# Performance work log

Measured on AMD Instinct MI355X. Metric: run time of the kernel, lower is better.

The kernel has to match this reference:

```python
import jax, jax.numpy as jnp
import numpy as np

N = 100000
E = 1600000
VOCAB = 16
D = 128   # node_embedding_dim == hidden_channels
NUM_LAYERS = 3


def setup_inputs() -> dict:
    key = jax.random.key(0)
    ks = jax.random.split(key, 12)
    x = jax.random.randint(ks[0], (N, 1), 0, VOCAB, dtype=jnp.int64) if jax.config.jax_enable_x64 else jax.random.randint(ks[0], (N, 1), 0, VOCAB, dtype=jnp.int32)
    edge_index = jax.random.randint(ks[1], (2, E), 0, N, dtype=jnp.int32)
    s = 1.0 / np.sqrt(D)
    inp = {
        "x": x,
        "edge_index": edge_index,
        "emb": jax.random.normal(ks[2], (VOCAB, D), jnp.float32),
        "W0": jax.random.normal(ks[3], (D, D), jnp.float32) * s,
        "b0": jnp.zeros((D,), jnp.float32),
        "W1": jax.random.normal(ks[4], (D, D), jnp.float32) * s,
        "b1": jnp.zeros((D,), jnp.float32),
        "W2": jax.random.normal(ks[5], (D, D), jnp.float32) * s,
        "b2": jnp.zeros((D,), jnp.float32),
        "Wm1": jax.random.normal(ks[6], (2 * D, D), jnp.float32) * (1.0 / np.sqrt(2 * D)),
        "bm1": jnp.zeros((D,), jnp.float32),
        "Wm2": jax.random.normal(ks[7], (D, 3), jnp.float32) * s,
        "bm2": jnp.zeros((3,), jnp.float32),
    }
    return inp


def _gcn_conv(h, src_sl, dst_sl, norm, W, b):
    # PyG GCNConv: x' = scatter_dst(norm * (x W)[src]) + b, with self-loops included
    hW = h @ W                                   # [N, D]
    msg = hW[src_sl] * norm[:, None]             # [(E+N), D] gather
    agg = jax.ops.segment_sum(msg, dst_sl, num_segments=N)  # scatter-add
    return agg + b


def reference(x, edge_index, emb, W0, b0, W1, b1, W2, b2, Wm1, bm1, Wm2, bm2):
    src, dst = edge_index[0], edge_index[1]
    # add self-loops
    loop = jnp.arange(N, dtype=src.dtype)
    src_sl = jnp.concatenate([src, loop])
    dst_sl = jnp.concatenate([dst, loop])
    # symmetric degree normalization: deg counted on dst (col)
    deg = jax.ops.segment_sum(jnp.ones_like(dst_sl, jnp.float32), dst_sl, num_segments=N)
    dis = jnp.where(deg > 0, jax.lax.rsqrt(jnp.maximum(deg, 1.0)), 0.0)
    norm = dis[src_sl] * dis[dst_sl]             # [(E+N)]

    # node encoder: embedding lookup (dropout omitted: eval mode)
    h = emb[x[:, 0]]                             # [N, D]
    for W, b in ((W0, b0), (W1, b1), (W2, b2)):
        h = jax.nn.relu(_gcn_conv(h, src_sl, dst_sl, norm, W, b))

    # edge classifier: gather endpoints, concat, MLP
    ef = jnp.concatenate([h[src], h[dst]], axis=-1)   # [E, 2D]
    hid = jax.nn.relu(ef @ Wm1 + bm1)
    return hid @ Wm2 + bm2                             # [E, 3]
```

## Files before the change

kernel.cpp:

```cpp
#include <hip/hip_runtime.h>
#include <hip/hip_bf16.h>

#define N_NODES 100000
#define N_EDGES 1600000


__global__ void zero_cnt_k(int* cnt, int n) {
    int i = blockIdx.x * 256 + threadIdx.x;
    if (i < n) cnt[i] = 0;
}

__global__ void hist_k(const int* __restrict__ ei, int* __restrict__ cnt, int E) {
    int e = blockIdx.x * 256 + threadIdx.x;
    if (e < E) atomicAdd(&cnt[ei[E + e]], 1);
}

__global__ void dis_k(const int* __restrict__ cnt, const int* __restrict__ x,
                      float* __restrict__ dis, float2* __restrict__ sx, int n) {
    int i = blockIdx.x * 256 + threadIdx.x;
    if (i < n) {
        float d = rsqrtf(1.0f + (float)cnt[i]);
        dis[i] = d;
        sx[i] = make_float2(d, __int_as_float(x[i]));
    }
}

__global__ void scan_cnt_k(const int* __restrict__ cnt, int* __restrict__ offs,
                           int* __restrict__ bsum, int n) {
    __shared__ int buf[2][256];
    int t = threadIdx.x;
    int i = blockIdx.x * 256 + t;
    int v = (i < n) ? cnt[i] : 0;
    int p = 0;
    buf[0][t] = v;
    __syncthreads();
    for (int off = 1; off < 256; off <<= 1) {
        int nv = buf[p][t];
        if (t >= off) nv += buf[p][t - off];
        buf[p ^ 1][t] = nv;
        p ^= 1;
        __syncthreads();
    }
    if (i < n) offs[i] = buf[p][t] - v;
    if (t == 255) bsum[blockIdx.x] = buf[p][t];
}

__global__ void scan_bsum_k(int* __restrict__ bsum, int nb) {
    __shared__ int buf[2][512];
    int t = threadIdx.x;
    int v = (t < nb) ? bsum[t] : 0;
    int p = 0;
    buf[0][t] = v;
    __syncthreads();
    for (int off = 1; off < 512; off <<= 1) {
        int nv = buf[p][t];
        if (t >= off) nv += buf[p][t - off];
        buf[p ^ 1][t] = nv;
        p ^= 1;
        __syncthreads();
    }
    if (t < nb) bsum[t] = buf[p][t] - v;
}

__global__ void scan_add_k(int* __restrict__ offs, int* __restrict__ cursor,
                           const int* __restrict__ bsum, int n, int total) {
    int i = blockIdx.x * 256 + threadIdx.x;
    if (i < n) {
        int o = offs[i] + bsum[blockIdx.x];
        offs[i] = o;
        cursor[i] = o;
    }
    if (i == 0) offs[n] = total;
}

__global__ void fill_csr_k(const int* __restrict__ ei, int* __restrict__ cursor,
                           int* __restrict__ srcs, int* __restrict__ eid, int E) {
    int e = blockIdx.x * 256 + threadIdx.x;
    if (e < E) {
        int s = ei[e];
        int d = ei[E + e];
        int pos = atomicAdd(&cursor[d], 1);
        srcs[pos] = s;
        eid[pos] = e;
    }
}


__global__ void t0_k(const float* __restrict__ emb, const float* __restrict__ W0,
                     float* __restrict__ T0) {
    int v = blockIdx.x;
    int c = threadIdx.x;
    float acc = 0.f;
    for (int k = 0; k < 128; ++k) acc += emb[v * 128 + k] * W0[k * 128 + c];
    T0[v * 128 + c] = acc;
}

__global__ __launch_bounds__(256) void vgather_k(const float2* __restrict__ sx,
                                                 const int* __restrict__ offs,
                                                 const int* __restrict__ srcs,
                                                 const float* __restrict__ dis,
                                                 const int* __restrict__ x,
                                                 const float* __restrict__ T0,
                                                 const float* __restrict__ b0,
                                                 float* __restrict__ h, int n) {
    __shared__ float t0s[16 * 128];
    __shared__ float cv[4][16];
    int t = threadIdx.x;
    #pragma unroll
    for (int i = 0; i < 8; ++i) t0s[t + i * 256] = T0[t + i * 256];
    if (t < 64) cv[t >> 4][t & 15] = 0.f;
    __syncthreads();

    int w = t >> 6, lane = t & 63;
    int node = blockIdx.x * 4 + w;
    float di = dis[node];
    int j0 = offs[node], j1 = offs[node + 1];
    for (int j = j0 + lane; j < j1; j += 64) {
        float2 v = sx[srcs[j]];
        atomicAdd(&cv[w][__float_as_int(v.y)], v.x);
    }
    if (lane == 0) atomicAdd(&cv[w][x[node]], di);
    __syncthreads();

    float2 acc = make_float2(0.f, 0.f);
    #pragma unroll
    for (int v = 0; v < 16; ++v) {
        float c = cv[w][v];
        float2 tv = *(const float2*)&t0s[v * 128 + lane * 2];
        acc.x += c * tv.x;
        acc.y += c * tv.y;
    }
    float2 bb = *(const float2*)&b0[lane * 2];
    float2 r = make_float2(fmaxf(di * acc.x + bb.x, 0.f),
                           fmaxf(di * acc.y + bb.y, 0.f));
    ((float2*)h)[(size_t)node * 64 + lane] = r;
}


__global__ __launch_bounds__(256) void matmul128_k(const float* __restrict__ in,
                                                   const float* __restrict__ W,
                                                   float* __restrict__ out,
                                                   const float* __restrict__ scale,
                                                   int n) {
    __shared__ float hlds[64][132];
    int t = threadIdx.x;
    int row0 = blockIdx.x * 64;
    #pragma unroll
    for (int it = 0; it < 8; ++it) {
        int i4 = t + it * 256;
        int r = i4 >> 5, c4 = (i4 & 31) << 2;
        float4 v = make_float4(0.f, 0.f, 0.f, 0.f);
        int g = row0 + r;
        if (g < n) v = *(const float4*)&in[(size_t)g * 128 + c4];
        *(float4*)&hlds[r][c4] = v;
    }
    __syncthreads();
    int cg = t & 31, rg = t >> 5;
    int c0 = cg << 2;
    float acc[8][4];
    #pragma unroll
    for (int r = 0; r < 8; ++r)
        for (int j = 0; j < 4; ++j) acc[r][j] = 0.f;
    #pragma unroll 4
    for (int k = 0; k < 128; ++k) {
        float4 w = *(const float4*)&W[(size_t)k * 128 + c0];
        #pragma unroll
        for (int r = 0; r < 8; ++r) {
            float hk = hlds[rg * 8 + r][k];
            acc[r][0] += hk * w.x;
            acc[r][1] += hk * w.y;
            acc[r][2] += hk * w.z;
            acc[r][3] += hk * w.w;
        }
    }
    #pragma unroll
    for (int r = 0; r < 8; ++r) {
        int g = row0 + rg * 8 + r;
        if (g < n) {
            float sc = scale[g];
            float4 o = make_float4(acc[r][0] * sc, acc[r][1] * sc,
                                   acc[r][2] * sc, acc[r][3] * sc);
            *(float4*)&out[(size_t)g * 128 + c0] = o;
        }
    }
}

__global__ __launch_bounds__(256) void matmulAB_k(const float* __restrict__ in,
                                                  const float* __restrict__ WA,
                                                  const float* __restrict__ WB,
                                                  float* __restrict__ outA,
                                                  float* __restrict__ outB, int n) {
    __shared__ float hlds[64][132];
    int t = threadIdx.x;
    int row0 = blockIdx.x * 64;
    #pragma unroll
    for (int it = 0; it < 8; ++it) {
        int i4 = t + it * 256;
        int r = i4 >> 5, c4 = (i4 & 31) << 2;
        float4 v = make_float4(0.f, 0.f, 0.f, 0.f);
        int g = row0 + r;
        if (g < n) v = *(const float4*)&in[(size_t)g * 128 + c4];
        *(float4*)&hlds[r][c4] = v;
    }
    __syncthreads();
    int cg = t & 31, rg = t >> 5;
    int c0 = cg << 2;
    float accA[8][4], accB[8][4];
    #pragma unroll
    for (int r = 0; r < 8; ++r)
        for (int j = 0; j < 4; ++j) { accA[r][j] = 0.f; accB[r][j] = 0.f; }
    #pragma unroll 2
    for (int k = 0; k < 128; ++k) {
        float4 wa = *(const float4*)&WA[(size_t)k * 128 + c0];
        float4 wb = *(const float4*)&WB[(size_t)k * 128 + c0];
        #pragma unroll
        for (int r = 0; r < 8; ++r) {
            float hk = hlds[rg * 8 + r][k];
            accA[r][0] += hk * wa.x;
            accA[r][1] += hk * wa.y;
            accA[r][2] += hk * wa.z;
            accA[r][3] += hk * wa.w;
            accB[r][0] += hk * wb.x;
            accB[r][1] += hk * wb.y;
            accB[r][2] += hk * wb.z;
            accB[r][3] += hk * wb.w;
        }
    }
    #pragma unroll
    for (int r = 0; r < 8; ++r) {
        int g = row0 + rg * 8 + r;
        if (g < n) {
            *(float4*)&outA[(size_t)g * 128 + c0] = *(float4*)&accA[r][0];
            *(float4*)&outB[(size_t)g * 128 + c0] = *(float4*)&accB[r][0];
        }
    }
}

__global__ __launch_bounds__(256) void gcn_gather_k(const float* __restrict__ hW,
                                                    const int* __restrict__ offs,
                                                    const int* __restrict__ srcs,
                                                    const float* __restrict__ dis,
                                                    const float* __restrict__ bias,
                                                    float* __restrict__ hout, int n) {
    int t = threadIdx.x;
    int node = blockIdx.x * 4 + (t >> 6);
    int lane = t & 63;
    int g = lane >> 4, sl = lane & 15;
    const float4* hw4 = (const float4*)hW;
    float4 a0 = make_float4(0.f, 0.f, 0.f, 0.f), a1 = a0;
    if (g == 0) {
        size_t rb = (size_t)node * 32 + sl * 2;
        a0 = hw4[rb];
        a1 = hw4[rb + 1];
    }
    int j0 = offs[node], j1 = offs[node + 1];
    for (int j = j0 + g; j < j1; j += 4) {
        size_t rb = (size_t)srcs[j] * 32 + sl * 2;
        float4 u0 = hw4[rb], u1 = hw4[rb + 1];
        a0.x += u0.x; a0.y += u0.y; a0.z += u0.z; a0.w += u0.w;
        a1.x += u1.x; a1.y += u1.y; a1.z += u1.z; a1.w += u1.w;
    }
    #pragma unroll
    for (int m = 16; m <= 32; m <<= 1) {
        a0.x += __shfl_xor(a0.x, m); a0.y += __shfl_xor(a0.y, m);
        a0.z += __shfl_xor(a0.z, m); a0.w += __shfl_xor(a0.w, m);
        a1.x += __shfl_xor(a1.x, m); a1.y += __shfl_xor(a1.y, m);
        a1.z += __shfl_xor(a1.z, m); a1.w += __shfl_xor(a1.w, m);
    }
    if (g == 0) {
        float di = dis[node];
        float4 bb0 = *(const float4*)&bias[sl * 8];
        float4 bb1 = *(const float4*)&bias[sl * 8 + 4];
        float4 r0 = make_float4(fmaxf(di * a0.x + bb0.x, 0.f),
                                fmaxf(di * a0.y + bb0.y, 0.f),
                                fmaxf(di * a0.z + bb0.z, 0.f),
                                fmaxf(di * a0.w + bb0.w, 0.f));
        float4 r1 = make_float4(fmaxf(di * a1.x + bb1.x, 0.f),
                                fmaxf(di * a1.y + bb1.y, 0.f),
                                fmaxf(di * a1.z + bb1.z, 0.f),
                                fmaxf(di * a1.w + bb1.w, 0.f));
        size_t rb = (size_t)node * 32 + sl * 2;
        ((float4*)hout)[rb] = r0;
        ((float4*)hout)[rb + 1] = r1;
    }
}

__global__ __launch_bounds__(256) void edge_mlp_k(const int* __restrict__ offs,
                                                  const int* __restrict__ srcs,
                                                  const int* __restrict__ eid,
                                                  const float* __restrict__ A,
                                                  const float* __restrict__ B,
                                                  const float* __restrict__ Wm2,
                                                  const float* __restrict__ bm1,
                                                  const float* __restrict__ bm2,
                                                  float* __restrict__ out, int n) {
    int t = threadIdx.x;
    int node = blockIdx.x * 4 + (t >> 6);
    int lane = t & 63;
    int g = lane >> 4, sl = lane & 15;
    int j0 = offs[node], j1 = offs[node + 1];
    if (j0 == j1) return;

    const float4* B4 = (const float4*)(B + (size_t)node * 128 + sl * 8);
    const float4* bm14 = (const float4*)(bm1 + sl * 8);
    float4 pre0 = B4[0], pre1 = B4[1];
    float4 m0 = bm14[0], m1 = bm14[1];
    pre0.x += m0.x; pre0.y += m0.y; pre0.z += m0.z; pre0.w += m0.w;
    pre1.x += m1.x; pre1.y += m1.y; pre1.z += m1.z; pre1.w += m1.w;

    float wv[8][3];
    #pragma unroll
    for (int i = 0; i < 8; ++i) {
        int f = sl * 8 + i;
        wv[i][0] = Wm2[f * 3 + 0];
        wv[i][1] = Wm2[f * 3 + 1];
        wv[i][2] = Wm2[f * 3 + 2];
    }
    float c0 = bm2[0], c1 = bm2[1], c2 = bm2[2];

    for (int jb = j0; jb < j1; jb += 4) {
        int jj = jb + g;
        bool act = jj < j1;
        int jsafe = act ? jj : j0;
        int s = srcs[jsafe];
        int e = eid[jsafe];
        const float4* A4 = (const float4*)(A + (size_t)s * 128 + sl * 8);
        float4 a0 = A4[0], a1 = A4[1];
        float h[8];
        h[0] = fmaxf(a0.x + pre0.x, 0.f);
        h[1] = fmaxf(a0.y + pre0.y, 0.f);
        h[2] = fmaxf(a0.z + pre0.z, 0.f);
        h[3] = fmaxf(a0.w + pre0.w, 0.f);
        h[4] = fmaxf(a1.x + pre1.x, 0.f);
        h[5] = fmaxf(a1.y + pre1.y, 0.f);
        h[6] = fmaxf(a1.z + pre1.z, 0.f);
        h[7] = fmaxf(a1.w + pre1.w, 0.f);
        float p0 = 0.f, p1 = 0.f, p2 = 0.f;
        #pragma unroll
        for (int i = 0; i < 8; ++i) {
            p0 += h[i] * wv[i][0];
            p1 += h[i] * wv[i][1];
            p2 += h[i] * wv[i][2];
        }
        #pragma unroll
        for (int m = 1; m <= 8; m <<= 1) {
            p0 += __shfl_xor(p0, m);
            p1 += __shfl_xor(p1, m);
            p2 += __shfl_xor(p2, m);
        }
        if (act && sl == 0) {
            out[(size_t)e * 3 + 0] = p0 + c0;
            out[(size_t)e * 3 + 1] = p1 + c1;
            out[(size_t)e * 3 + 2] = p2 + c2;
        }
    }
}

extern "C" void kernel_launch(void* const* d_in, const int* in_sizes, int n_in,
                              void* d_out, int out_size, void* d_ws, size_t ws_size,
                              hipStream_t stream) {
    const int N = N_NODES, E = N_EDGES;
    const int* x    = (const int*)d_in[0];
    const int* ei   = (const int*)d_in[1];
    const float* emb = (const float*)d_in[2];
    const float* W0 = (const float*)d_in[3];
    const float* b0 = (const float*)d_in[4];
    const float* W1 = (const float*)d_in[5];
    const float* b1 = (const float*)d_in[6];
    const float* W2 = (const float*)d_in[7];
    const float* b2 = (const float*)d_in[8];
    const float* Wm1 = (const float*)d_in[9];
    const float* bm1 = (const float*)d_in[10];
    const float* Wm2 = (const float*)d_in[11];
    const float* bm2 = (const float*)d_in[12];
    float* out = (float*)d_out;

    char* p = (char*)d_ws;
    auto alloc = [&](size_t bytes) {
        char* r = p;
        p += (bytes + 511) & ~(size_t)511;
        return r;
    };
    int*    cnt    = (int*)alloc((size_t)N * 4);
    float*  dis    = (float*)alloc((size_t)N * 4);
    float2* sx     = (float2*)alloc((size_t)N * 8);
    int*    offs   = (int*)alloc((size_t)(N + 1) * 4);
    int*    cursor = (int*)alloc((size_t)N * 4);
    int*    bsum   = (int*)alloc(512 * 4);
    int*    srcs   = (int*)alloc((size_t)E * 4);
    int*    eid    = (int*)alloc((size_t)E * 4);
    float*  T0     = (float*)alloc(16 * 128 * 4);
    float*  buf0   = (float*)alloc((size_t)N * 128 * 4);
    float*  buf1   = (float*)alloc((size_t)N * 128 * 4);
    float*  buf2   = (float*)alloc((size_t)N * 128 * 4);

    int nbN = (N + 255) / 256;
    int nbE = (E + 255) / 256;
    int nodeBlocks = N / 4;
    int mmBlocks = (N + 63) / 64;

    zero_cnt_k<<<nbN, 256, 0, stream>>>(cnt, N);
    hist_k<<<nbE, 256, 0, stream>>>(ei, cnt, E);
    dis_k<<<nbN, 256, 0, stream>>>(cnt, x, dis, sx, N);
    scan_cnt_k<<<nbN, 256, 0, stream>>>(cnt, offs, bsum, N);
    scan_bsum_k<<<1, 512, 0, stream>>>(bsum, nbN);
    scan_add_k<<<nbN, 256, 0, stream>>>(offs, cursor, bsum, N, E);
    fill_csr_k<<<nbE, 256, 0, stream>>>(ei, cursor, srcs, eid, E);

    t0_k<<<16, 128, 0, stream>>>(emb, W0, T0);
    vgather_k<<<nodeBlocks, 256, 0, stream>>>(sx, offs, srcs, dis, x, T0, b0, buf0, N);

    const float* Ws[2] = {W1, W2};
    const float* bs[2] = {b1, b2};
    for (int l = 0; l < 2; ++l) {
        matmul128_k<<<mmBlocks, 256, 0, stream>>>(buf0, Ws[l], buf1, dis, N);
        gcn_gather_k<<<nodeBlocks, 256, 0, stream>>>(buf1, offs, srcs, dis, bs[l], buf0, N);
    }

    matmulAB_k<<<mmBlocks, 256, 0, stream>>>(buf0, Wm1, Wm1 + 128 * 128, buf1, buf2, N);

    edge_mlp_k<<<nodeBlocks, 256, 0, stream>>>(offs, srcs, eid, buf1, buf2, Wm2, bm1, bm2, out, N);
}
```

Baseline: 819.9 us.

## Fuse degree-norm into scan, vectorize matmul k-loop, widen gather edge parallelism

Folds the degree-normalization kernel into the count scan kernel, which removes one launch and one pass over the counts. The two dense matmul kernels now read four k-rows of the weights and a float4 of the LDS row per step, cutting the number of LDS loads. The GCN gather now splits each wavefront into 8 edge groups of 8 lanes, with each lane holding four float4 accumulators. This gives more edges in flight per node, at the cost of more registers and an extra shuffle-reduction step.

```diff
diff --git a/kernel.cpp b/kernel.cpp
--- a/kernel.cpp
+++ b/kernel.cpp
@@ -15,22 +15,18 @@
     if (e < E) atomicAdd(&cnt[ei[E + e]], 1);
 }
 
-__global__ void dis_k(const int* __restrict__ cnt, const int* __restrict__ x,
-                      float* __restrict__ dis, float2* __restrict__ sx, int n) {
-    int i = blockIdx.x * 256 + threadIdx.x;
+__global__ void scan_cnt_k(const int* __restrict__ cnt, const int* __restrict__ x,
+                           int* __restrict__ offs, int* __restrict__ bsum,
+                           float* __restrict__ dis, float2* __restrict__ sx, int n) {
+    __shared__ int buf[2][256];
+    int t = threadIdx.x;
+    int i = blockIdx.x * 256 + t;
+    int v = (i < n) ? cnt[i] : 0;
     if (i < n) {
-        float d = rsqrtf(1.0f + (float)cnt[i]);
+        float d = rsqrtf(1.0f + (float)v);
         dis[i] = d;
         sx[i] = make_float2(d, __int_as_float(x[i]));
     }
-}
-
-__global__ void scan_cnt_k(const int* __restrict__ cnt, int* __restrict__ offs,
-                           int* __restrict__ bsum, int n) {
-    __shared__ int buf[2][256];
-    int t = threadIdx.x;
-    int i = blockIdx.x * 256 + t;
-    int v = (i < n) ? cnt[i] : 0;
     int p = 0;
     buf[0][t] = v;
     __syncthreads();
@@ -162,15 +158,18 @@
     for (int r = 0; r < 8; ++r)
         for (int j = 0; j < 4; ++j) acc[r][j] = 0.f;
     #pragma unroll 4
-    for (int k = 0; k < 128; ++k) {
-        float4 w = *(const float4*)&W[(size_t)k * 128 + c0];
+    for (int kc = 0; kc < 32; ++kc) {
+        float4 w0 = *(const float4*)&W[(size_t)(4 * kc + 0) * 128 + c0];
+        float4 w1 = *(const float4*)&W[(size_t)(4 * kc + 1) * 128 + c0];
+        float4 w2 = *(const float4*)&W[(size_t)(4 * kc + 2) * 128 + c0];
+        float4 w3 = *(const float4*)&W[(size_t)(4 * kc + 3) * 128 + c0];
         #pragma unroll
         for (int r = 0; r < 8; ++r) {
-            float hk = hlds[rg * 8 + r][k];
-            acc[r][0] += hk * w.x;
-            acc[r][1] += hk * w.y;
-            acc[r][2] += hk * w.z;
-            acc[r][3] += hk * w.w;
+            float4 hv = *(const float4*)&hlds[rg * 8 + r][kc * 4];
+            acc[r][0] += hv.x * w0.x + hv.y * w1.x + hv.z * w2.x + hv.w * w3.x;
+            acc[r][1] += hv.x * w0.y + hv.y * w1.y + hv.z * w2.y + hv.w * w3.y;
+            acc[r][2] += hv.x * w0.z + hv.y * w1.z + hv.z * w2.z + hv.w * w3.z;
+            acc[r][3] += hv.x * w0.w + hv.y * w1.w + hv.z * w2.w + hv.w * w3.w;
         }
     }
     #pragma unroll
@@ -210,20 +209,26 @@
     for (int r = 0; r < 8; ++r)
         for (int j = 0; j < 4; ++j) { accA[r][j] = 0.f; accB[r][j] = 0.f; }
     #pragma unroll 2
-    for (int k = 0; k < 128; ++k) {
-        float4 wa = *(const float4*)&WA[(size_t)k * 128 + c0];
-        float4 wb = *(const float4*)&WB[(size_t)k * 128 + c0];
+    for (int kc = 0; kc < 32; ++kc) {
+        float4 wa0 = *(const float4*)&WA[(size_t)(4 * kc + 0) * 128 + c0];
+        float4 wa1 = *(const float4*)&WA[(size_t)(4 * kc + 1) * 128 + c0];
+        float4 wa2 = *(const float4*)&WA[(size_t)(4 * kc + 2) * 128 + c0];
+        float4 wa3 = *(const float4*)&WA[(size_t)(4 * kc + 3) * 128 + c0];
+        float4 wb0 = *(const float4*)&WB[(size_t)(4 * kc + 0) * 128 + c0];
+        float4 wb1 = *(const float4*)&WB[(size_t)(4 * kc + 1) * 128 + c0];
+        float4 wb2 = *(const float4*)&WB[(size_t)(4 * kc + 2) * 128 + c0];
+        float4 wb3 = *(const float4*)&WB[(size_t)(4 * kc + 3) * 128 + c0];
         #pragma unroll
         for (int r = 0; r < 8; ++r) {
-            float hk = hlds[rg * 8 + r][k];
-            accA[r][0] += hk * wa.x;
-            accA[r][1] += hk * wa.y;
-            accA[r][2] += hk * wa.z;
-            accA[r][3] += hk * wa.w;
-            accB[r][0] += hk * wb.x;
-            accB[r][1] += hk * wb.y;
-            accB[r][2] += hk * wb.z;
-            accB[r][3] += hk * wb.w;
+            float4 hv = *(const float4*)&hlds[rg * 8 + r][kc * 4];
+            accA[r][0] += hv.x * wa0.x + hv.y * wa1.x + hv.z * wa2.x + hv.w * wa3.x;
+            accA[r][1] += hv.x * wa0.y + hv.y * wa1.y + hv.z * wa2.y + hv.w * wa3.y;
+            accA[r][2] += hv.x * wa0.z + hv.y * wa1.z + hv.z * wa2.z + hv.w * wa3.z;
+            accA[r][3] += hv.x * wa0.w + hv.y * wa1.w + hv.z * wa2.w + hv.w * wa3.w;
+            accB[r][0] += hv.x * wb0.x + hv.y * wb1.x + hv.z * wb2.x + hv.w * wb3.x;
+            accB[r][1] += hv.x * wb0.y + hv.y * wb1.y + hv.z * wb2.y + hv.w * wb3.y;
+            accB[r][2] += hv.x * wb0.z + hv.y * wb1.z + hv.z * wb2.z + hv.w * wb3.z;
+            accB[r][3] += hv.x * wb0.w + hv.y * wb1.w + hv.z * wb2.w + hv.w * wb3.w;
         }
     }
     #pragma unroll
@@ -245,43 +250,47 @@
     int t = threadIdx.x;
     int node = blockIdx.x * 4 + (t >> 6);
     int lane = t & 63;
-    int g = lane >> 4, sl = lane & 15;
+    int g = lane >> 3, sl = lane & 7;
     const float4* hw4 = (const float4*)hW;
-    float4 a0 = make_float4(0.f, 0.f, 0.f, 0.f), a1 = a0;
+    size_t selfrb = (size_t)node * 32 + sl;
+    float4 a[4];
     if (g == 0) {
-        size_t rb = (size_t)node * 32 + sl * 2;
-        a0 = hw4[rb];
-        a1 = hw4[rb + 1];
+        #pragma unroll
+        for (int k = 0; k < 4; ++k) a[k] = hw4[selfrb + 8 * k];
+    } else {
+        #pragma unroll
+        for (int k = 0; k < 4; ++k) a[k] = make_float4(0.f, 0.f, 0.f, 0.f);
     }
     int j0 = offs[node], j1 = offs[node + 1];
-    for (int j = j0 + g; j < j1; j += 4) {
-        size_t rb = (size_t)srcs[j] * 32 + sl * 2;
-        float4 u0 = hw4[rb], u1 = hw4[rb + 1];
-        a0.x += u0.x; a0.y += u0.y; a0.z += u0.z; a0.w += u0.w;
-        a1.x += u1.x; a1.y += u1.y; a1.z += u1.z; a1.w += u1.w;
-    }
-    #pragma unroll
-    for (int m = 16; m <= 32; m <<= 1) {
-        a0.x += __shfl_xor(a0.x, m); a0.y += __shfl_xor(a0.y, m);
-        a0.z += __shfl_xor(a0.z, m); a0.w += __shfl_xor(a0.w, m);
-        a1.x += __shfl_xor(a1.x, m); a1.y += __shfl_xor(a1.y, m);
-        a1.z += __shfl_xor(a1.z, m); a1.w += __shfl_xor(a1.w, m);
+    for (int j = j0 + g; j < j1; j += 8) {
+        size_t rb = (size_t)srcs[j] * 32 + sl;
+        #pragma unroll
+        for (int k = 0; k < 4; ++k) {
+            float4 u = hw4[rb + 8 * k];
+            a[k].x += u.x; a[k].y += u.y; a[k].z += u.z; a[k].w += u.w;
+        }
+    }
+    #pragma unroll
+    for (int m = 8; m <= 32; m <<= 1) {
+        #pragma unroll
+        for (int k = 0; k < 4; ++k) {
+            a[k].x += __shfl_xor(a[k].x, m);
+            a[k].y += __shfl_xor(a[k].y, m);
+            a[k].z += __shfl_xor(a[k].z, m);
+            a[k].w += __shfl_xor(a[k].w, m);
+        }
     }
     if (g == 0) {
         float di = dis[node];
-        float4 bb0 = *(const float4*)&bias[sl * 8];
-        float4 bb1 = *(const float4*)&bias[sl * 8 + 4];
-        float4 r0 = make_float4(fmaxf(di * a0.x + bb0.x, 0.f),
-                                fmaxf(di * a0.y + bb0.y, 0.f),
-                                fmaxf(di * a0.z + bb0.z, 0.f),
-                                fmaxf(di * a0.w + bb0.w, 0.f));
-        float4 r1 = make_float4(fmaxf(di * a1.x + bb1.x, 0.f),
-                                fmaxf(di * a1.y + bb1.y, 0.f),
-                                fmaxf(di * a1.z + bb1.z, 0.f),
-                                fmaxf(di * a1.w + bb1.w, 0.f));
-        size_t rb = (size_t)node * 32 + sl * 2;
-        ((float4*)hout)[rb] = r0;
-        ((float4*)hout)[rb + 1] = r1;
+        #pragma unroll
+        for (int k = 0; k < 4; ++k) {
+            float4 bb = ((const float4*)bias)[sl + 8 * k];
+            float4 r = make_float4(fmaxf(di * a[k].x + bb.x, 0.f),
+                                   fmaxf(di * a[k].y + bb.y, 0.f),
+                                   fmaxf(di * a[k].z + bb.z, 0.f),
+                                   fmaxf(di * a[k].w + bb.w, 0.f));
+            ((float4*)hout)[selfrb + 8 * k] = r;
+        }
     }
 }
 
@@ -401,8 +410,7 @@
 
     zero_cnt_k<<<nbN, 256, 0, stream>>>(cnt, N);
     hist_k<<<nbE, 256, 0, stream>>>(ei, cnt, E);
-    dis_k<<<nbN, 256, 0, stream>>>(cnt, x, dis, sx, N);
-    scan_cnt_k<<<nbN, 256, 0, stream>>>(cnt, offs, bsum, N);
+    scan_cnt_k<<<nbN, 256, 0, stream>>>(cnt, x, offs, bsum, dis, sx, N);
     scan_bsum_k<<<1, 512, 0, stream>>>(bsum, nbN);
     scan_add_k<<<nbN, 256, 0, stream>>>(offs, cursor, bsum, N, E);
     fill_csr_k<<<nbE, 256, 0, stream>>>(ei, cursor, srcs, eid, E);
```

After: 854.1 us. +4.2%, slower.
